# Optimization experiments

Measured on AMD Instinct MI355X. Metric: run time of the kernel, lower is better.

The kernel has to match this reference:

```python
import jax, jax.numpy as jnp
import numpy as np

B, T, C = 2, 2048, 1024
N_HEAD = 16
HEAD_DIM = C // N_HEAD
ROPE_BASE = 10000.0


def setup_inputs() -> dict:
    key = jax.random.key(0)
    ks = jax.random.split(key, 5)
    s = 0.02
    return {
        "x": jax.random.normal(ks[0], (B, T, C), dtype=jnp.float32),
        "Wq": jax.random.normal(ks[1], (C, C), dtype=jnp.float32) * s,
        "Wk": jax.random.normal(ks[2], (C, C), dtype=jnp.float32) * s,
        "Wv": jax.random.normal(ks[3], (C, C), dtype=jnp.float32) * s,
        "Wo": jax.random.normal(ks[4], (C, C), dtype=jnp.float32) * s,
    }


def _rope_cos_sin(seq_len, head_dim, dtype):
    inv_freq = 1.0 / (ROPE_BASE ** (jnp.arange(0, head_dim, 2, dtype=jnp.float32) / head_dim))
    t = jnp.arange(seq_len, dtype=jnp.float32)
    freqs = jnp.einsum("i,j->ij", t, inv_freq)          # [T, head_dim/2]
    emb = jnp.concatenate([freqs, freqs], axis=-1)        # [T, head_dim]
    return jnp.cos(emb).astype(dtype), jnp.sin(emb).astype(dtype)


def _rotate_half(x):
    x1, x2 = jnp.split(x, 2, axis=-1)
    return jnp.concatenate([-x2, x1], axis=-1)


def _mha(x, Wq, Wk, Wv, Wo):
    b, t, c = x.shape
    # torch nn.Linear stores weight [out, in]: y = x @ W.T
    q = (x @ Wq.T).reshape(b, t, N_HEAD, HEAD_DIM).transpose(0, 2, 1, 3)  # [B,H,T,D]
    k = (x @ Wk.T).reshape(b, t, N_HEAD, HEAD_DIM).transpose(0, 2, 1, 3)
    v = (x @ Wv.T).reshape(b, t, N_HEAD, HEAD_DIM).transpose(0, 2, 1, 3)
    cos, sin = _rope_cos_sin(t, HEAD_DIM, x.dtype)        # [T,D] each, broadcast over B,H
    q = q * cos + _rotate_half(q) * sin
    k = k * cos + _rotate_half(k) * sin
    scale = 1.0 / np.sqrt(HEAD_DIM).astype(np.float32)
    att = jnp.einsum("bhqd,bhkd->bhqk", q, k) * scale     # [B,H,T,T]
    causal = jnp.tril(jnp.ones((t, t), dtype=bool))
    att = jnp.where(causal, att, jnp.finfo(att.dtype).min)
    att = jax.nn.softmax(att, axis=-1)
    y = jnp.einsum("bhqk,bhkd->bhqd", att, v)             # [B,H,T,D]
    y = y.transpose(0, 2, 1, 3).reshape(b, t, c)
    return y @ Wo.T


def reference(x, Wq, Wk, Wv, Wo):
    return _mha(x, Wq, Wk, Wv, Wo)
```

## Files before the change

### kernel.cpp

```cpp
#include <hip/hip_runtime.h>

#define BB 2
#define TT 2048
#define CC 1024
#define NH 16
#define HD 64

typedef __attribute__((ext_vector_type(8))) short bf16x8;
typedef __attribute__((ext_vector_type(4))) float floatx4;
typedef __attribute__((ext_vector_type(16))) float floatx16;

__device__ __forceinline__ unsigned short f2bf(float f) {
    union { float f; unsigned int u; } v; v.f = f;
    unsigned int u = v.u;
    u = (u + 0x7fffu + ((u >> 16) & 1u)) >> 16;
    return (unsigned short)u;
}
__device__ __forceinline__ float bf2f(unsigned short u) {
    return __uint_as_float((unsigned)u << 16);
}

typedef __attribute__((address_space(3))) unsigned char* lds_ptr_t;
typedef const __attribute__((address_space(1))) unsigned char* glob_ptr_t;
__device__ __forceinline__ void gll16(const void* g, void* l) {
    __builtin_amdgcn_global_load_lds((glob_ptr_t)g, (lds_ptr_t)l, 16, 0, 0);
}

__global__ __launch_bounds__(256) void cast_all_k(const float* __restrict__ x,
                                                  const float* __restrict__ wq,
                                                  const float* __restrict__ wk,
                                                  const float* __restrict__ wv,
                                                  const float* __restrict__ wo,
                                                  unsigned short* __restrict__ xb,
                                                  unsigned short* __restrict__ wqkvb,
                                                  unsigned short* __restrict__ wob,
                                                  float2* __restrict__ tabQ,
                                                  float2* __restrict__ tabK) {
    if (blockIdx.x >= 8192) {
        int idx = (blockIdx.x - 8192) * 256 + threadIdx.x;
        int t = idx >> 5, j = idx & 31;
        const float C1 = 0.41524101186092f;
        const float I2PI = 0.15915494309189535f;
        float rev = (float)t * (__builtin_amdgcn_exp2f(-(float)j * C1) * I2PI);
        rev -= floorf(rev);
        float ang = rev * 6.2831853071796f;
        float c = __cosf(ang), s = __sinf(ang);
        const float qs = 0.18033688011112f;
        tabK[idx] = make_float2(c, s);
        tabQ[idx] = make_float2(c * qs, s * qs);
        return;
    }
    int i = blockIdx.x * 256 + threadIdx.x;
    const float* src;
    unsigned short* dst;
    if (i < 1048576) {
        src = x + (size_t)i * 4;
        dst = xb + (size_t)i * 4;
    } else {
        int w   = (i - 1048576) >> 18;
        int off = (i - 1048576) & 262143;
        const float* s0 = (w == 0) ? wq : (w == 1) ? wk : (w == 2) ? wv : wo;
        unsigned short* d0 = (w == 3) ? wob : (wqkvb + (size_t)w * 1048576);
        src = s0 + (size_t)off * 4;
        dst = d0 + (size_t)off * 4;
    }
    float4 v = *(const float4*)src;
    ushort4 o;
    o.x = f2bf(v.x); o.y = f2bf(v.y); o.z = f2bf(v.z); o.w = f2bf(v.w);
    *(ushort4*)dst = o;
}

__global__ __launch_bounds__(256, 2) void gemm_o_k(const unsigned short* __restrict__ A,
                                                   const unsigned short* __restrict__ Bt,
                                                   float* __restrict__ C, int N, int K) {
    __shared__ __align__(16) unsigned short As[128][64];
    __shared__ __align__(16) unsigned short Bs[64][64];
    const int tid  = threadIdx.x;
    const int wave = tid >> 6;
    const int lane = tid & 63;
    const int quad = lane >> 4;
    const int l16  = lane & 15;
    const int sw   = l16 & 7;
    const int wr = (wave >> 1) * 64;
    const int wc = (wave & 1) * 32;
    const int bid = blockIdx.x;
    const int xcd = bid & 7, sl = bid >> 3;
    const int row0 = (xcd * 4 + (sl >> 4)) * 128;
    const int col0 = (sl & 15) * 64;
    const int w8r = wave * 8 + (lane >> 3);
    const int cg  = ((lane & 7) ^ (lane >> 3)) * 8;
    const int cl  = (lane & 7) * 8;

    const unsigned short* Ap = A  + (size_t)(row0 + w8r) * K + cg;
    const unsigned short* Bp = Bt + (size_t)(col0 + w8r) * K + cg;

    floatx4 acc[4][2];
    #pragma unroll
    for (int i = 0; i < 4; i++)
        #pragma unroll
        for (int j = 0; j < 2; j++) acc[i][j] = (floatx4){0.f, 0.f, 0.f, 0.f};

    for (int k0 = 0; k0 < K; k0 += 64) {
        __syncthreads();
        #pragma unroll
        for (int isu = 0; isu < 4; isu++)
            gll16(Ap + (size_t)(isu * 32) * K + k0, &As[isu * 32 + w8r][cl]);
        #pragma unroll
        for (int isu = 0; isu < 2; isu++)
            gll16(Bp + (size_t)(isu * 32) * K + k0, &Bs[isu * 32 + w8r][cl]);
        __syncthreads();
        #pragma unroll
        for (int kk = 0; kk < 2; kk++) {
            bf16x8 af[4], bfr[2];
            #pragma unroll
            for (int i = 0; i < 4; i++)
                af[i]  = *(const bf16x8*)&As[wr + 16 * i + l16][((kk * 4 + quad) ^ sw) * 8];
            #pragma unroll
            for (int j = 0; j < 2; j++)
                bfr[j] = *(const bf16x8*)&Bs[wc + 16 * j + l16][((kk * 4 + quad) ^ sw) * 8];
            #pragma unroll
            for (int i = 0; i < 4; i++)
                #pragma unroll
                for (int j = 0; j < 2; j++)
                    acc[i][j] = __builtin_amdgcn_mfma_f32_16x16x32_bf16(af[i], bfr[j], acc[i][j], 0, 0, 0);
        }
    }

    #pragma unroll
    for (int i = 0; i < 4; i++)
        #pragma unroll
        for (int j = 0; j < 2; j++)
            #pragma unroll
            for (int r = 0; r < 4; r++) {
                int row = row0 + wr + 16 * i + quad * 4 + r;
                int col = col0 + wc + 16 * j + l16;
                C[(size_t)row * N + col] = acc[i][j][r];
            }
}

__global__ __launch_bounds__(256) void gemm_qkv_k(const unsigned short* __restrict__ A,
                                                  const unsigned short* __restrict__ Bt,
                                                  const float2* __restrict__ tabQ,
                                                  const float2* __restrict__ tabK,
                                                  unsigned short* __restrict__ Qb,
                                                  unsigned short* __restrict__ Kb,
                                                  unsigned short* __restrict__ Vb) {
    __shared__ __align__(16) unsigned short SMEM[128 * 128];
    unsigned short (*As)[64] = (unsigned short(*)[64])SMEM;
    unsigned short (*Bs)[64] = (unsigned short(*)[64])(SMEM + 128 * 64);
    unsigned short (*Eb)[128] = (unsigned short(*)[128])SMEM;
    const int K = 1024;
    const int tid  = threadIdx.x;
    const int wave = tid >> 6;
    const int lane = tid & 63;
    const int quad = lane >> 4;
    const int l16  = lane & 15;
    const int sw   = l16 & 7;
    const int wr = (wave >> 1) * 64;
    const int wc = (wave & 1) * 64;
    const int bid = blockIdx.x;
    const int xcd = bid & 7, sl = bid >> 3;
    const int row0 = (xcd * 4 + sl / 24) * 128;
    const int col0 = (sl % 24) * 128;
    const int w8r = wave * 8 + (lane >> 3);
    const int cg  = ((lane & 7) ^ (lane >> 3)) * 8;
    const int cl  = (lane & 7) * 8;

    const unsigned short* Ap = A  + (size_t)(row0 + w8r) * K + cg;
    const unsigned short* Bp = Bt + (size_t)(col0 + w8r) * K + cg;

    floatx4 acc[4][4];
    #pragma unroll
    for (int i = 0; i < 4; i++)
        #pragma unroll
        for (int j = 0; j < 4; j++) acc[i][j] = (floatx4){0.f, 0.f, 0.f, 0.f};

    for (int k0 = 0; k0 < K; k0 += 64) {
        __syncthreads();
        #pragma unroll
        for (int isu = 0; isu < 4; isu++) {
            gll16(Ap + (size_t)(isu * 32) * K + k0, &As[isu * 32 + w8r][cl]);
            gll16(Bp + (size_t)(isu * 32) * K + k0, &Bs[isu * 32 + w8r][cl]);
        }
        __syncthreads();
        #pragma unroll
        for (int kk = 0; kk < 2; kk++) {
            bf16x8 af[4], bfr[4];
            #pragma unroll
            for (int i = 0; i < 4; i++)
                af[i]  = *(const bf16x8*)&As[wr + 16 * i + l16][((kk * 4 + quad) ^ sw) * 8];
            #pragma unroll
            for (int j = 0; j < 4; j++)
                bfr[j] = *(const bf16x8*)&Bs[wc + 16 * j + l16][((kk * 4 + quad) ^ sw) * 8];
            #pragma unroll
            for (int i = 0; i < 4; i++)
                #pragma unroll
                for (int j = 0; j < 4; j++)
                    acc[i][j] = __builtin_amdgcn_mfma_f32_16x16x32_bf16(af[i], bfr[j], acc[i][j], 0, 0, 0);
        }
    }

    __syncthreads();
    #pragma unroll
    for (int i = 0; i < 4; i++)
        #pragma unroll
        for (int j = 0; j < 4; j++)
            #pragma unroll
            for (int r = 0; r < 4; r++) {
                int erow = wr + 16 * i + quad * 4 + r;
                int col  = wc + 16 * j + l16;
                int pcol = (((col >> 3) ^ (erow & 15)) << 3) | (col & 7);
                Eb[erow][pcol] = f2bf(acc[i][j][r]);
            }
    __syncthreads();

    const int row  = tid >> 1;
    const int half = tid & 1;
    const int grow = row0 + row;
    const int t    = grow & (TT - 1);
    const int bb   = grow >> 11;
    const int sect = col0 >> 10;
    const int hh   = ((col0 & 1023) >> 6) + half;
    union { int4 q[8]; unsigned short u[64]; } raw;
    #pragma unroll
    for (int i = 0; i < 8; i++) {
        int pg = (half * 8 + i) ^ (row & 15);
        raw.q[i] = *(const int4*)&Eb[row][pg << 3];
    }
    size_t obase = ((size_t)(bb * NH + hh) * TT + t) * 64;
    if (sect == 2) {
        #pragma unroll
        for (int i = 0; i < 8; i++) *(int4*)(Vb + obase + 8 * i) = raw.q[i];
    } else {
        const float4* tab = (const float4*)((sect ? tabK : tabQ) + (size_t)t * 32);
        unsigned short* dst = sect ? Kb : Qb;
        union { int4 q[8]; unsigned short u[64]; } o;
        #pragma unroll
        for (int i = 0; i < 16; i++) {
            float4 cs = tab[i];
            int j0 = 2 * i, j1 = 2 * i + 1;
            float a0 = bf2f(raw.u[j0]), b0 = bf2f(raw.u[j0 + 32]);
            float a1 = bf2f(raw.u[j1]), b1 = bf2f(raw.u[j1 + 32]);
            o.u[j0]      = f2bf(a0 * cs.x - b0 * cs.y);
            o.u[j0 + 32] = f2bf(b0 * cs.x + a0 * cs.y);
            o.u[j1]      = f2bf(a1 * cs.z - b1 * cs.w);
            o.u[j1 + 32] = f2bf(b1 * cs.z + a1 * cs.w);
        }
        #pragma unroll
        for (int i = 0; i < 8; i++) *(int4*)(dst + obase + 8 * i) = o.q[i];
    }
}

__global__ __launch_bounds__(256) void vtr_k(const unsigned short* __restrict__ Vb,
                                             unsigned short* __restrict__ Vt) {
    __shared__ __align__(16) unsigned short Vsh[64][70];
    const int tid = threadIdx.x;
    const int tt = blockIdx.x;
    const int bh = blockIdx.y;
    const int sr = tid >> 2;
    const int sc = (tid & 3) * 16;
    const unsigned short* src = Vb + ((size_t)bh * TT + tt * 64 + sr) * 64 + sc;
    *(int4*)&Vsh[sr][sc]     = *(const int4*)src;
    *(int4*)&Vsh[sr][sc + 8] = *(const int4*)(src + 8);
    __syncthreads();
    const int dr = tid >> 2;
    const int tc = (tid & 3) * 16;
    unsigned short tv[16];
    #pragma unroll
    for (int i = 0; i < 16; i++) {
        int x = tc + i;
        int key = (x & ~15) + (x & 3) + ((x >> 2) & 1) * 8 + ((x >> 3) & 1) * 4;
        tv[i] = Vsh[key][dr];
    }
    size_t vo = ((size_t)bh * 64 + dr) * TT + tt * 64 + tc;
    *(int4*)(Vt + vo)     = *(int4*)&tv[0];
    *(int4*)(Vt + vo + 8) = *(int4*)&tv[8];
}

__global__ __launch_bounds__(256, 4) void flash_k(const unsigned short* __restrict__ Qb,
                                                  const unsigned short* __restrict__ Kb,
                                                  const unsigned short* __restrict__ Vt,
                                                  unsigned short* __restrict__ Yb) {
    __shared__ __align__(16) unsigned short Ks[2][64][72];
    __shared__ __align__(16) unsigned short Vs[2][64][72];
    const int tid  = threadIdx.x;
    const int wave = tid >> 6;
    const int lane = tid & 63;
    const int h    = lane >> 5;
    const int l32  = lane & 31;
    const int g    = wave >> 1;
    const int s    = wave & 1;
    const int j    = blockIdx.x >> 5;
    const int qj   = (j < 16) ? (31 - j) : (j - 16);
    const int bh   = blockIdx.x & 31;
    const int q0   = qj * 64;
    const int qw   = q0 + g * 32 + l32;
    const int nt   = qj + 1;
    const int n0   = (nt + 1) >> 1;
    const int n1   = nt - n0;
    const int sr = tid >> 2;
    const int sc = (tid & 3) * 16;

    bf16x8 qf[4];
    {
        const unsigned short* qp = Qb + ((size_t)bh * TT + qw) * 64 + h * 8;
        #pragma unroll
        for (int kk = 0; kk < 4; kk++) qf[kk] = *(const bf16x8*)(qp + kk * 16);
    }

    floatx16 accO[2];
    accO[0] = (floatx16)(0.f);
    accO[1] = (floatx16)(0.f);
    float lsum = 0.f;

    const unsigned short* kbase = Kb + (size_t)bh * TT * 64;
    const unsigned short* vbase = Vt + (size_t)bh * 64 * TT;

    int4 ka0, kb0, va0, vb0, ka1, kb1, va1, vb1;
    {
        const unsigned short* kp = kbase + (size_t)sr * 64 + sc;
        const unsigned short* vp = vbase + (size_t)sr * TT + sc;
        ka0 = *(const int4*)kp; kb0 = *(const int4*)(kp + 8);
        va0 = *(const int4*)vp; vb0 = *(const int4*)(vp + 8);
        if (n1 > 0) {
            const unsigned short* kp1 = kbase + ((size_t)(n0 * 64) + sr) * 64 + sc;
            const unsigned short* vp1 = vbase + (size_t)sr * TT + n0 * 64 + sc;
            ka1 = *(const int4*)kp1; kb1 = *(const int4*)(kp1 + 8);
            va1 = *(const int4*)vp1; vb1 = *(const int4*)(vp1 + 8);
        }
    }

    for (int i = 0; i < n0; i++) {
        __syncthreads();
        *(int4*)&Ks[0][sr][sc]     = ka0;
        *(int4*)&Ks[0][sr][sc + 8] = kb0;
        *(int4*)&Vs[0][sr][sc]     = va0;
        *(int4*)&Vs[0][sr][sc + 8] = vb0;
        if (i < n1) {
            *(int4*)&Ks[1][sr][sc]     = ka1;
            *(int4*)&Ks[1][sr][sc + 8] = kb1;
            *(int4*)&Vs[1][sr][sc]     = va1;
            *(int4*)&Vs[1][sr][sc + 8] = vb1;
        }
        __syncthreads();
        if (i + 1 < n0) {
            const unsigned short* kp = kbase + ((size_t)((i + 1) * 64) + sr) * 64 + sc;
            const unsigned short* vp = vbase + (size_t)sr * TT + (i + 1) * 64 + sc;
            ka0 = *(const int4*)kp; kb0 = *(const int4*)(kp + 8);
            va0 = *(const int4*)vp; vb0 = *(const int4*)(vp + 8);
            if (i + 1 < n1) {
                const unsigned short* kp1 = kbase + ((size_t)((n0 + i + 1) * 64) + sr) * 64 + sc;
                const unsigned short* vp1 = vbase + (size_t)sr * TT + (n0 + i + 1) * 64 + sc;
                ka1 = *(const int4*)kp1; kb1 = *(const int4*)(kp1 + 8);
                va1 = *(const int4*)vp1; vb1 = *(const int4*)(vp1 + 8);
            }
        }

        const int kt = (s ? n0 : 0) + i;
        const bool active = (s == 0) || (i < n1);
        if (active) {
            const bool diag = (kt == qj);
            bf16x8 pfrag[4];

            #pragma unroll
            for (int mb = 0; mb < 2; mb++) {
                floatx16 sacc = (floatx16)(0.f);
                __builtin_amdgcn_s_setprio(1);
                #pragma unroll
                for (int kk = 0; kk < 4; kk++) {
                    bf16x8 kf = *(const bf16x8*)&Ks[s][32 * mb + l32][kk * 16 + h * 8];
                    sacc = __builtin_amdgcn_mfma_f32_32x32x16_bf16(kf, qf[kk], sacc, 0, 0, 0);
                }
                __builtin_amdgcn_s_setprio(0);
                float p[16];
                const int kmb = kt * 64 + 32 * mb + 4 * h;
                #pragma unroll
                for (int r = 0; r < 16; r++) {
                    float pv = __builtin_amdgcn_exp2f(sacc[r]);
                    if (diag) {
                        int ki = kmb + (r & 3) + 8 * (r >> 2);
                        if (ki > qw) pv = 0.f;
                    }
                    lsum += pv;
                    p[r] = pv;
                }
                #pragma unroll
                for (int half = 0; half < 2; half++) {
                    union { bf16x8 v; unsigned u[4]; } pk;
                    #pragma unroll
                    for (int i2 = 0; i2 < 4; i2++) {
                        unsigned ulo = __float_as_uint(p[half * 8 + 2 * i2]);
                        unsigned uhi = __float_as_uint(p[half * 8 + 2 * i2 + 1]);
                        pk.u[i2] = (ulo >> 16) | (uhi & 0xffff0000u);
                    }
                    pfrag[2 * mb + half] = pk.v;
                }
            }

            __builtin_amdgcn_s_setprio(1);
            #pragma unroll
            for (int mbo = 0; mbo < 2; mbo++) {
                #pragma unroll
                for (int kk = 0; kk < 4; kk++) {
                    bf16x8 vf = *(const bf16x8*)&Vs[s][32 * mbo + l32][kk * 16 + h * 8];
                    accO[mbo] = __builtin_amdgcn_mfma_f32_32x32x16_bf16(vf, pfrag[kk], accO[mbo], 0, 0, 0);
                }
            }
            __builtin_amdgcn_s_setprio(0);
        }
    }

    lsum += __shfl_xor(lsum, 32);
    __syncthreads();
    float* Fb = (float*)&Ks[0][0][0];
    float* Lb = (float*)&Vs[0][0][0];
    if (s == 1) {
        float* f = Fb + (size_t)(g * 32 + l32) * 65;
        #pragma unroll
        for (int mbo = 0; mbo < 2; mbo++)
            #pragma unroll
            for (int a = 0; a < 4; a++) {
                int d0 = 32 * mbo + 8 * a + 4 * h;
                f[d0 + 0] = accO[mbo][4 * a + 0];
                f[d0 + 1] = accO[mbo][4 * a + 1];
                f[d0 + 2] = accO[mbo][4 * a + 2];
                f[d0 + 3] = accO[mbo][4 * a + 3];
            }
        if (lane < 32) Lb[g * 32 + l32] = lsum;
    }
    __syncthreads();
    if (s == 0) {
        const float* f = Fb + (size_t)(g * 32 + l32) * 65;
        const float inv = 1.0f / (lsum + Lb[g * 32 + l32]);
        const int bb = bh >> 4, hh = bh & 15;
        unsigned short* orow = Yb + ((size_t)(bb * TT + qw)) * CC + hh * 64;
        #pragma unroll
        for (int mbo = 0; mbo < 2; mbo++)
            #pragma unroll
            for (int a = 0; a < 4; a++) {
                int d0 = 32 * mbo + 8 * a + 4 * h;
                ushort4 o4;
                o4.x = f2bf((accO[mbo][4 * a + 0] + f[d0 + 0]) * inv);
                o4.y = f2bf((accO[mbo][4 * a + 1] + f[d0 + 1]) * inv);
                o4.z = f2bf((accO[mbo][4 * a + 2] + f[d0 + 2]) * inv);
                o4.w = f2bf((accO[mbo][4 * a + 3] + f[d0 + 3]) * inv);
                *(ushort4*)(orow + d0) = o4;
            }
    }
}

extern "C" void kernel_launch(void* const* d_in, const int* in_sizes, int n_in,
                              void* d_out, int out_size, void* d_ws, size_t ws_size,
                              hipStream_t stream) {
    (void)in_sizes; (void)n_in; (void)out_size; (void)ws_size;
    const float* x  = (const float*)d_in[0];
    const float* Wq = (const float*)d_in[1];
    const float* Wk = (const float*)d_in[2];
    const float* Wv = (const float*)d_in[3];
    const float* Wo = (const float*)d_in[4];
    float* out = (float*)d_out;
    char* ws = (char*)d_ws;

    unsigned short* xb    = (unsigned short*)(ws + 0);
    unsigned short* wqkvb = (unsigned short*)(ws + (8ull  << 20));
    unsigned short* wob   = (unsigned short*)(ws + (14ull << 20));
    unsigned short* Qb    = (unsigned short*)(ws + (16ull << 20));
    unsigned short* Kb    = (unsigned short*)(ws + (24ull << 20));
    unsigned short* Vb    = (unsigned short*)(ws + (32ull << 20));
    unsigned short* Vt    = (unsigned short*)(ws + (40ull << 20));
    unsigned short* Yb    = (unsigned short*)(ws + (48ull << 20));
    float2* tabQ = (float2*)(ws + (73ull << 20));
    float2* tabK = (float2*)(ws + (73ull << 20) + (512ull << 10));

    cast_all_k<<<8448, 256, 0, stream>>>(x, Wq, Wk, Wv, Wo, xb, wqkvb, wob, tabQ, tabK);
    gemm_qkv_k<<<768, 256, 0, stream>>>(xb, wqkvb, tabQ, tabK, Qb, Kb, Vb);
    vtr_k<<<dim3(32, 32), 256, 0, stream>>>(Vb, Vt);
    flash_k<<<1024, 256, 0, stream>>>(Qb, Kb, Vt, Yb);
    gemm_o_k<<<512, 256, 0, stream>>>(Yb, wob, out, 1024, 1024);
}
```

Measured before the change: 173.9 us.

## Load K/V tiles directly to LDS with XOR-swizzled layout

Replaces the register-staged prefetch of K and V tiles with direct global-to-LDS loads (gll16) into a compact unpadded buffer. An XOR swizzle on the 16-byte column groups takes over from the row padding to avoid bank conflicts on the MFMA fragment reads. This frees the VGPRs that held the prefetched tiles and removes the explicit LDS store step. In exchange, the loads are no longer issued one iteration ahead, so load latency is exposed before the barrier each iteration.

Result: no change. 172.5 us (-0.8%).

```diff
diff --git a/kernel.cpp b/kernel.cpp
--- a/kernel.cpp
+++ b/kernel.cpp
@@ -281,8 +281,7 @@
                                                   const unsigned short* __restrict__ Kb,
                                                   const unsigned short* __restrict__ Vt,
                                                   unsigned short* __restrict__ Yb) {
-    __shared__ __align__(16) unsigned short Ks[2][64][72];
-    __shared__ __align__(16) unsigned short Vs[2][64][72];
+    __shared__ __align__(16) unsigned short SMEM[2][2][64][64];
     const int tid  = threadIdx.x;
     const int wave = tid >> 6;
     const int lane = tid & 63;
@@ -298,8 +297,11 @@
     const int nt   = qj + 1;
     const int n0   = (nt + 1) >> 1;
     const int n1   = nt - n0;
-    const int sr = tid >> 2;
-    const int sc = (tid & 3) * 16;
+    const int l8  = lane >> 3;
+    const int lg  = lane & 7;
+    const int srow = wave * 8 + l8;
+    const int sgr  = lg ^ l8;
+    const int xr   = l32 & 7;
 
     bf16x8 qf[4];
     {
@@ -316,45 +318,23 @@
     const unsigned short* kbase = Kb + (size_t)bh * TT * 64;
     const unsigned short* vbase = Vt + (size_t)bh * 64 * TT;
 
-    int4 ka0, kb0, va0, vb0, ka1, kb1, va1, vb1;
-    {
-        const unsigned short* kp = kbase + (size_t)sr * 64 + sc;
-        const unsigned short* vp = vbase + (size_t)sr * TT + sc;
-        ka0 = *(const int4*)kp; kb0 = *(const int4*)(kp + 8);
-        va0 = *(const int4*)vp; vb0 = *(const int4*)(vp + 8);
-        if (n1 > 0) {
-            const unsigned short* kp1 = kbase + ((size_t)(n0 * 64) + sr) * 64 + sc;
-            const unsigned short* vp1 = vbase + (size_t)sr * TT + n0 * 64 + sc;
-            ka1 = *(const int4*)kp1; kb1 = *(const int4*)(kp1 + 8);
-            va1 = *(const int4*)vp1; vb1 = *(const int4*)(vp1 + 8);
-        }
-    }
-
     for (int i = 0; i < n0; i++) {
         __syncthreads();
-        *(int4*)&Ks[0][sr][sc]     = ka0;
-        *(int4*)&Ks[0][sr][sc + 8] = kb0;
-        *(int4*)&Vs[0][sr][sc]     = va0;
-        *(int4*)&Vs[0][sr][sc + 8] = vb0;
+        #pragma unroll
+        for (int c = 0; c < 2; c++) {
+            int r = 32 * c + srow;
+            gll16(kbase + ((size_t)(i * 64) + r) * 64 + sgr * 8, &SMEM[0][0][r][lg * 8]);
+            gll16(vbase + (size_t)r * TT + i * 64 + sgr * 8,     &SMEM[1][0][r][lg * 8]);
+        }
         if (i < n1) {
-            *(int4*)&Ks[1][sr][sc]     = ka1;
-            *(int4*)&Ks[1][sr][sc + 8] = kb1;
-            *(int4*)&Vs[1][sr][sc]     = va1;
-            *(int4*)&Vs[1][sr][sc + 8] = vb1;
-        }
-        __syncthreads();
-        if (i + 1 < n0) {
-            const unsigned short* kp = kbase + ((size_t)((i + 1) * 64) + sr) * 64 + sc;
-            const unsigned short* vp = vbase + (size_t)sr * TT + (i + 1) * 64 + sc;
-            ka0 = *(const int4*)kp; kb0 = *(const int4*)(kp + 8);
-            va0 = *(const int4*)vp; vb0 = *(const int4*)(vp + 8);
-            if (i + 1 < n1) {
-                const unsigned short* kp1 = kbase + ((size_t)((n0 + i + 1) * 64) + sr) * 64 + sc;
-                const unsigned short* vp1 = vbase + (size_t)sr * TT + (n0 + i + 1) * 64 + sc;
-                ka1 = *(const int4*)kp1; kb1 = *(const int4*)(kp1 + 8);
-                va1 = *(const int4*)vp1; vb1 = *(const int4*)(vp1 + 8);
-            }
-        }
+            #pragma unroll
+            for (int c = 0; c < 2; c++) {
+                int r = 32 * c + srow;
+                gll16(kbase + ((size_t)((n0 + i) * 64) + r) * 64 + sgr * 8, &SMEM[0][1][r][lg * 8]);
+                gll16(vbase + (size_t)r * TT + (n0 + i) * 64 + sgr * 8,     &SMEM[1][1][r][lg * 8]);
+            }
+        }
+        __syncthreads();
 
         const int kt = (s ? n0 : 0) + i;
         const bool active = (s == 0) || (i < n1);
@@ -368,7 +348,7 @@
                 __builtin_amdgcn_s_setprio(1);
                 #pragma unroll
                 for (int kk = 0; kk < 4; kk++) {
-                    bf16x8 kf = *(const bf16x8*)&Ks[s][32 * mb + l32][kk * 16 + h * 8];
+                    bf16x8 kf = *(const bf16x8*)&SMEM[0][s][32 * mb + l32][((2 * kk + h) ^ xr) * 8];
                     sacc = __builtin_amdgcn_mfma_f32_32x32x16_bf16(kf, qf[kk], sacc, 0, 0, 0);
                 }
                 __builtin_amdgcn_s_setprio(0);
@@ -402,7 +382,7 @@
             for (int mbo = 0; mbo < 2; mbo++) {
                 #pragma unroll
                 for (int kk = 0; kk < 4; kk++) {
-                    bf16x8 vf = *(const bf16x8*)&Vs[s][32 * mbo + l32][kk * 16 + h * 8];
+                    bf16x8 vf = *(const bf16x8*)&SMEM[1][s][32 * mbo + l32][((2 * kk + h) ^ xr) * 8];
                     accO[mbo] = __builtin_amdgcn_mfma_f32_32x32x16_bf16(vf, pfrag[kk], accO[mbo], 0, 0, 0);
                 }
             }
@@ -412,8 +392,8 @@
 
     lsum += __shfl_xor(lsum, 32);
     __syncthreads();
-    float* Fb = (float*)&Ks[0][0][0];
-    float* Lb = (float*)&Vs[0][0][0];
+    float* Fb = (float*)&SMEM[0][0][0][0];
+    float* Lb = Fb + 64 * 65;
     if (s == 1) {
         float* f = Fb + (size_t)(g * 32 + l32) * 65;
         #pragma unroll
```
